# Kernel tuning notes

Measured on AMD Instinct MI355X. Metric: run time of the kernel, lower is better.

Reference implementation:

```python
import jax, jax.numpy as jnp
import numpy as np


def _lstm_dir(x_tbd, Wx, Wh, b, reverse):
    # x_tbd: [T, B, D]; Wx: [D, 4H]; Wh: [H, 4H]; b: [4H]
    if reverse:
        x_tbd = x_tbd[::-1]
    pre = jnp.einsum('tbd,dk->tbk', x_tbd, Wx) + b  # precompute input projection
    T, B, _ = x_tbd.shape
    H = Wh.shape[0]
    init = (jnp.zeros((B, H), x_tbd.dtype), jnp.zeros((B, H), x_tbd.dtype))

    def step(carry, zt):
        c, h = carry
        z = zt + h @ Wh  # [B, 4H]
        i, f, g, o = jnp.split(z, 4, axis=-1)
        i = jax.nn.sigmoid(i)
        f = jax.nn.sigmoid(f)
        g = jnp.tanh(g)
        o = jax.nn.sigmoid(o)
        c = f * c + i * g
        h = o * jnp.tanh(c)
        return (c, h), h

    _, hs = jax.lax.scan(step, init, pre)  # hs: [T, B, H]
    if reverse:
        hs = hs[::-1]
    return hs


def _bilstm(x, layers):
    # x: [B, T, D] batch-major -> time-major
    x = jnp.swapaxes(x, 0, 1)  # [T, B, D]
    for (Wxf, Whf, bf, Wxb, Whb, bb) in layers:
        hf = _lstm_dir(x, Wxf, Whf, bf, reverse=False)
        hb = _lstm_dir(x, Wxb, Whb, bb, reverse=True)
        x = jnp.concatenate([hf, hb], axis=-1)  # [T, B, 2H]
    return jnp.swapaxes(x, 0, 1)  # [B, T, 2H]


def setup_inputs() -> dict:
    key = jax.random.key(0)
    B, T, D, H = 8, 2048, 512, 512
    ks = jax.random.split(key, 9)
    s_in = 1.0 / np.sqrt(D)
    s_h = 1.0 / np.sqrt(H)
    s_in2 = 1.0 / np.sqrt(2 * H)
    return {
        'x': jax.random.normal(ks[0], (B, T, D), jnp.float32),
        'Wx0f': jax.random.normal(ks[1], (D, 4 * H), jnp.float32) * s_in,
        'Wh0f': jax.random.normal(ks[2], (H, 4 * H), jnp.float32) * s_h,
        'b0f': jnp.zeros((4 * H,), jnp.float32),
        'Wx0b': jax.random.normal(ks[3], (D, 4 * H), jnp.float32) * s_in,
        'Wh0b': jax.random.normal(ks[4], (H, 4 * H), jnp.float32) * s_h,
        'b0b': jnp.zeros((4 * H,), jnp.float32),
        'Wx1f': jax.random.normal(ks[5], (2 * H, 4 * H), jnp.float32) * s_in2,
        'Wh1f': jax.random.normal(ks[6], (H, 4 * H), jnp.float32) * s_h,
        'b1f': jnp.zeros((4 * H,), jnp.float32),
        'Wx1b': jax.random.normal(ks[7], (2 * H, 4 * H), jnp.float32) * s_in2,
        'Wh1b': jax.random.normal(ks[8], (H, 4 * H), jnp.float32) * s_h,
        'b1b': jnp.zeros((4 * H,), jnp.float32),
    }


def reference(x, Wx0f, Wh0f, b0f, Wx0b, Wh0b, b0b, Wx1f, Wh1f, b1f, Wx1b, Wh1b, b1b):
    layers = [
        (Wx0f, Wh0f, b0f, Wx0b, Wh0b, b0b),
        (Wx1f, Wh1f, b1f, Wx1b, Wh1b, b1b),
    ]
    return _bilstm(x, layers)
```

## Files before the change

### kernel.cpp

```cpp
#include <hip/hip_runtime.h>
#include <hip/hip_bf16.h>
#include <stdint.h>

typedef unsigned short u16;
typedef unsigned int   u32;
typedef unsigned long long u64;
typedef __attribute__((ext_vector_type(8))) short short8;
typedef __attribute__((ext_vector_type(4))) float f32x4;

#define T_SEQ 2048
#define NTOK  16384
#define NGATE 4096

__device__ __forceinline__ u16 f2bf(float f) {
    u32 u = __builtin_bit_cast(u32, f);
    return (u16)((u + 0x7fffu + ((u >> 16) & 1u)) >> 16);
}
__device__ __forceinline__ float bf2f(u16 s) {
    return __builtin_bit_cast(float, (u32)s << 16);
}

__device__ __forceinline__ void load2_sc0(const u64* p0, const u64* p1, u64& a, u64& b) {
    asm volatile("global_load_dwordx2 %0, %2, off sc0\n\t"
                 "global_load_dwordx2 %1, %3, off sc0\n\t"
                 "s_waitcnt vmcnt(0)"
                 : "=&v"(a), "=&v"(b)
                 : "v"(p0), "v"(p1)
                 : "memory");
}
__device__ __forceinline__ void store_sc0(u32* p, u32 v) {
    asm volatile("global_store_dword %0, %1, off sc0" :: "v"(p), "v"(v) : "memory");
}

__global__ void k_init(u32* comm, int n_comm) {
    int i = blockIdx.x * blockDim.x + threadIdx.x;
    int stride = gridDim.x * blockDim.x;
    for (int k = i; k < n_comm; k += stride) comm[k] = 0u;
}

__global__ void k_f2bf(const float* __restrict__ src, u16* __restrict__ dst, int n4) {
    int i = blockIdx.x * blockDim.x + threadIdx.x;
    if (i >= n4) return;
    float4 v = ((const float4*)src)[i];
    u32 lo = (u32)f2bf(v.x) | ((u32)f2bf(v.y) << 16);
    u32 hi = (u32)f2bf(v.z) | ((u32)f2bf(v.w) << 16);
    ((uint2*)dst)[i] = make_uint2(lo, hi);
}

__global__ void k_pack_wxT(const float* __restrict__ Wf, const float* __restrict__ Wb,
                           u16* __restrict__ dst, int K, int klog ) {
    int gid = blockIdx.x * blockDim.x + threadIdx.x;
    if (gid >= (NGATE << klog)) return;
    int n  = gid >> klog;
    int kc = gid & ((1 << klog) - 1);
    int dir = n >> 11, pcol = n & 2047;
    int c = pcol >> 4, uu = (pcol >> 2) & 3, g = pcol & 3;
    int u = c * 4 + uu;
    int oc = g * 512 + u;
    const float* src = dir ? Wb : Wf;
    u16* d = dst + (size_t)n * K + kc * 8;
    #pragma unroll
    for (int j = 0; j < 8; j++) d[j] = f2bf(src[(size_t)(kc * 8 + j) * 2048 + oc]);
}

__global__ void k_pack_whF(const float* __restrict__ Whf, const float* __restrict__ Whb,
                           u16* __restrict__ dst) {
    int gid = blockIdx.x * blockDim.x + threadIdx.x;
    int lane = gid & 63, kk = (gid >> 6) & 15, c = (gid >> 10) & 127, dir = (gid >> 17) & 1;
    int col16 = lane & 15, uu = col16 >> 2, g = col16 & 3;
    int u = c * 4 + uu, oc = g * 512 + u;
    int kbase = kk * 32 + (lane >> 4) * 8;
    const float* src = dir ? Whb : Whf;
    u16* d = dst + (size_t)gid * 8;
    #pragma unroll
    for (int j = 0; j < 8; j++) d[j] = f2bf(src[(size_t)(kbase + j) * 2048 + oc]);
}

template <int K>
__global__ __launch_bounds__(256) void k_gemm(const u16* __restrict__ A,
                                              const u16* __restrict__ BT,
                                              u16* __restrict__ C) {
    __shared__ __align__(16) u16 a_lds[128][72];
    __shared__ __align__(16) u16 b_lds[128][72];
    const int tid = threadIdx.x;
    const int lane = tid & 63;
    const int wav = tid >> 6;
    const int wr = wav >> 1, wc = wav & 1;
    const int row0 = blockIdx.y * 128, col0 = blockIdx.x * 128;
    const int r_ld = lane & 15;
    const int k_ld = (lane >> 4) * 8;
    f32x4 acc[4][4] = {};
    for (int kt = 0; kt < K; kt += 64) {
        __syncthreads();
        #pragma unroll
        for (int it = 0; it < 4; it++) {
            int cc = tid + it * 256;
            int r = cc >> 3, ko = (cc & 7) * 8;
            *(short8*)&a_lds[r][ko] = *(const short8*)&A[(size_t)(row0 + r) * K + kt + ko];
            *(short8*)&b_lds[r][ko] = *(const short8*)&BT[(size_t)(col0 + r) * K + kt + ko];
        }
        __syncthreads();
        #pragma unroll
        for (int kk = 0; kk < 2; kk++) {
            short8 af[4], bfr[4];
            #pragma unroll
            for (int m = 0; m < 4; m++)
                af[m] = *(const short8*)&a_lds[wr * 64 + m * 16 + r_ld][kk * 32 + k_ld];
            #pragma unroll
            for (int n = 0; n < 4; n++)
                bfr[n] = *(const short8*)&b_lds[wc * 64 + n * 16 + r_ld][kk * 32 + k_ld];
            #pragma unroll
            for (int m = 0; m < 4; m++)
                #pragma unroll
                for (int n = 0; n < 4; n++)
                    acc[m][n] = __builtin_amdgcn_mfma_f32_16x16x32_bf16(af[m], bfr[n], acc[m][n], 0, 0, 0);
        }
    }
    const int rrow = (lane >> 4) * 4;
    const int rcol = lane & 15;
    #pragma unroll
    for (int m = 0; m < 4; m++)
        #pragma unroll
        for (int n = 0; n < 4; n++) {
            size_t rbase = (size_t)(row0 + wr * 64 + m * 16 + rrow);
            int col = col0 + wc * 64 + n * 16 + rcol;
            #pragma unroll
            for (int r = 0; r < 4; r++)
                C[(rbase + r) * NGATE + col] = f2bf(acc[m][n][r]);
        }
}

__global__ __launch_bounds__(1024) void k_scan(
    const u16* __restrict__ pre,
    const u16* __restrict__ whF,
    const float* __restrict__ bias_f, const float* __restrict__ bias_b,
    u16* __restrict__ y_bf,
    float* __restrict__ y_f32,
    u32* __restrict__ commL,
    u32* __restrict__ commF)
{
    const int xcd = (int)(blockIdx.x & 7);
    if (xcd > 1) return;
    const int dir = xcd;
    const int p   = (int)(blockIdx.x >> 3);

    __shared__ __align__(16) u16   h_lds[2][8][520];
    __shared__ __align__(16) u16   z_pre[2][8][264];
    __shared__ __align__(16) float z_mm[2][8][260];

    const int tid = threadIdx.x;
    const int l   = tid & 63;
    const int w   = tid >> 6;

    short8 bfrag[16];
    {
        const u16* base = whF + (size_t)(dir * 128 + p * 16 + w) * 8192 + (size_t)l * 8;
        #pragma unroll
        for (int kk = 0; kk < 16; kk++) bfrag[kk] = *(const short8*)(base + kk * 512);
    }

    float c_st = 0.f;
    float bi = 0.f, bff = 0.f, bg = 0.f, bo = 0.f;
    const int gj  = tid & 63;
    const int u_g = p * 64 + gj;
    if (tid < 512) {
        const float* bias = dir ? bias_b : bias_f;
        bi  = bias[u_g];        bff = bias[512 + u_g];
        bg  = bias[1024 + u_g]; bo  = bias[1536 + u_g];
    }
    const int a_b = l & 7;
    const int a_k = (l >> 4) * 8;
    const int zr  = l >> 4;

    u32* const cbL = commL + (size_t)dir * 8192;
    u32* const cbF = commF + (size_t)dir * 8192;
    const int sb_b0 = tid >> 8;
    const int sb_u  = (2 * tid) & 511;

    for (int s = 0; s < T_SEQ; s++) {
        const int t  = dir ? (T_SEQ - 1 - s) : s;
        const int hb = s & 1;
        short8 preg;
        if (tid < 256) {
            int b = tid >> 5, seg = tid & 31;
            preg = *(const short8*)&pre[((size_t)b * T_SEQ + t) * NGATE + dir * 2048 + p * 256 + seg * 8];
        }
        asm volatile("" ::: "memory");
        {
            const u64* sbL = (const u64*)(cbL + (size_t)((s + 1) & 1) * 4096);
            const u64* sbF = (const u64*)(cbF + (size_t)((s + 1) & 1) * 4096);
            const u32 want = (u32)s & 0xffffu;
            u32 W0 = 0, W1 = 0, W2 = 0, W3 = 0;
            bool D0 = false, D1 = false, D2 = false, D3 = false;
            do {
                u64 l0 = __hip_atomic_load(&sbL[tid],        __ATOMIC_RELAXED, __HIP_MEMORY_SCOPE_AGENT);
                u64 l1 = __hip_atomic_load(&sbL[tid + 1024], __ATOMIC_RELAXED, __HIP_MEMORY_SCOPE_AGENT);
                u64 f0, f1;
                load2_sc0(&sbF[tid], &sbF[tid + 1024], f0, f1);
                if (!D0) { u32 a = (u32)f0;         u32 b = (u32)l0;
                           if ((a >> 16) == want) { W0 = a; D0 = true; }
                           else if ((b >> 16) == want) { W0 = b; D0 = true; } }
                if (!D1) { u32 a = (u32)(f0 >> 32); u32 b = (u32)(l0 >> 32);
                           if ((a >> 16) == want) { W1 = a; D1 = true; }
                           else if ((b >> 16) == want) { W1 = b; D1 = true; } }
                if (!D2) { u32 a = (u32)f1;         u32 b = (u32)l1;
                           if ((a >> 16) == want) { W2 = a; D2 = true; }
                           else if ((b >> 16) == want) { W2 = b; D2 = true; } }
                if (!D3) { u32 a = (u32)(f1 >> 32); u32 b = (u32)(l1 >> 32);
                           if ((a >> 16) == want) { W3 = a; D3 = true; }
                           else if ((b >> 16) == want) { W3 = b; D3 = true; } }
            } while (!(D0 && D1 && D2 && D3));
            *(u32*)&h_lds[hb][sb_b0][sb_u]     = (W0 & 0xffffu) | (W1 << 16);
            *(u32*)&h_lds[hb][sb_b0 + 4][sb_u] = (W2 & 0xffffu) | (W3 << 16);
        }
        if (tid < 256) {
            int b = tid >> 5, seg = tid & 31;
            *(short8*)&z_pre[hb][b][seg * 8] = preg;
        }
        __syncthreads();
        {
            f32x4 acc0 = {}, acc1 = {};
            #pragma unroll
            for (int kk = 0; kk < 8; kk++) {
                short8 a0 = *(const short8*)&h_lds[hb][a_b][kk * 32 + a_k];
                acc0 = __builtin_amdgcn_mfma_f32_16x16x32_bf16(a0, bfrag[kk], acc0, 0, 0, 0);
                short8 a1 = *(const short8*)&h_lds[hb][a_b][(kk + 8) * 32 + a_k];
                acc1 = __builtin_amdgcn_mfma_f32_16x16x32_bf16(a1, bfrag[kk + 8], acc1, 0, 0, 0);
            }
            if (zr < 2) {
                #pragma unroll
                for (int r = 0; r < 4; r++)
                    z_mm[hb][zr * 4 + r][w * 16 + (l & 15)] = acc0[r] + acc1[r];
            }
        }
        __syncthreads();
        if (tid < 512) {
            float4 z4 = *(const float4*)&z_mm[hb][w][4 * gj];
            u64 pz    = *(const u64*)&z_pre[hb][w][4 * gj];
            float zi = z4.x + bf2f((u16)pz)         + bi;
            float zf = z4.y + bf2f((u16)(pz >> 16)) + bff;
            float zg = z4.z + bf2f((u16)(pz >> 32)) + bg;
            float zo = z4.w + bf2f((u16)(pz >> 48)) + bo;
            float ig = 1.f / (1.f + __expf(-zi));
            float fg = 1.f / (1.f + __expf(-zf));
            float gg = 2.f / (1.f + __expf(-2.f * zg)) - 1.f;
            float og = 1.f / (1.f + __expf(-zo));
            c_st = fg * c_st + ig * gg;
            float th = 2.f / (1.f + __expf(-2.f * c_st)) - 1.f;
            float hv = og * th;
            u16 hb16 = f2bf(hv);
            u32 pw = (u32)hb16 | ((u32)((s + 1) & 0xffff) << 16);
            u32 idx = (u32)((s & 1) * 4096 + w * 512 + u_g);
            store_sc0(&cbF[idx], pw);
            __hip_atomic_store(&cbL[idx], pw, __ATOMIC_RELAXED, __HIP_MEMORY_SCOPE_AGENT);
            size_t rr = (size_t)w * T_SEQ + t;
            if (y_bf) y_bf[rr * 1024 + dir * 512 + u_g] = hb16;
            else      y_f32[rr * 1024 + dir * 512 + u_g] = hv;
        }
    }
}

extern "C" void kernel_launch(void* const* d_in, const int* in_sizes, int n_in,
                              void* d_out, int out_size, void* d_ws, size_t ws_size,
                              hipStream_t stream) {
    const float* x    = (const float*)d_in[0];
    const float* Wx0f = (const float*)d_in[1];
    const float* Wh0f = (const float*)d_in[2];
    const float* b0f  = (const float*)d_in[3];
    const float* Wx0b = (const float*)d_in[4];
    const float* Wh0b = (const float*)d_in[5];
    const float* b0b  = (const float*)d_in[6];
    const float* Wx1f = (const float*)d_in[7];
    const float* Wh1f = (const float*)d_in[8];
    const float* b1f  = (const float*)d_in[9];
    const float* Wx1b = (const float*)d_in[10];
    const float* Wh1b = (const float*)d_in[11];
    const float* b1b  = (const float*)d_in[12];
    float* out = (float*)d_out;

    char* ws = (char*)d_ws;
    size_t off = 0;
    auto take = [&](size_t bytes) {
        char* pp = ws + off;
        off = (off + bytes + 255) & ~(size_t)255;
        return pp;
    };
    u16* pre  = (u16*)take((size_t)NTOK * NGATE * 2);
    u16* x_bf = (u16*)take((size_t)NTOK * 512 * 2);
    u16* y0   = (u16*)take((size_t)NTOK * 1024 * 2);
    u16* wxT0 = (u16*)take((size_t)NGATE * 512 * 2);
    u16* wxT1 = (u16*)take((size_t)NGATE * 1024 * 2);
    u16* whF  = (u16*)take((size_t)2 * 2097152 * 2);
    u32* comm = (u32*)take((size_t)8 * 8192 * 4);

    u32* commL = comm;
    u32* commF = comm + 4 * 8192;

    k_init<<<32, 256, 0, stream>>>(comm, 8 * 8192);
    k_f2bf<<<8192, 256, 0, stream>>>(x, x_bf, NTOK * 512 / 4);
    k_pack_wxT<<<1024, 256, 0, stream>>>(Wx0f, Wx0b, wxT0, 512, 6);
    k_pack_wxT<<<2048, 256, 0, stream>>>(Wx1f, Wx1b, wxT1, 1024, 7);
    k_pack_whF<<<1024, 256, 0, stream>>>(Wh0f, Wh0b, whF);
    k_pack_whF<<<1024, 256, 0, stream>>>(Wh1f, Wh1b, whF + 2097152);

    k_gemm<512><<<dim3(32, 128), 256, 0, stream>>>(x_bf, wxT0, pre);
    k_scan<<<64, 1024, 0, stream>>>(pre, whF, b0f, b0b, y0, nullptr,
                                    commL, commF);
    k_gemm<1024><<<dim3(32, 128), 256, 0, stream>>>(y0, wxT1, pre);
    k_scan<<<64, 1024, 0, stream>>>(pre, whF + 2097152, b1f, b1b, nullptr, out,
                                    commL + 2 * 8192, commF + 2 * 8192);
}
```

Before: 11.99 ms.

## Split polling onto dedicated stager waves and poll mostly the sc0 buffer

Threads 512 to 1023 become dedicated stager waves. They alone poll the cross-block hidden-state exchange buffers and stage the precomputed gate inputs into LDS, while the lower threads handle gate math. Polling now reads four dwordx2 words per thread from the sc0 buffer each iteration and checks the atomic buffer only every 16th iteration. A pair of packed values counts as ready only when both halves carry the current step tag. The aim is to cut spin-loop memory traffic and take the exchange latency off the compute waves, at the cost of possibly slower detection when only the atomic copy is up to date.

```diff
diff --git a/kernel.cpp b/kernel.cpp
--- a/kernel.cpp
+++ b/kernel.cpp
@@ -20,12 +20,16 @@
     return __builtin_bit_cast(float, (u32)s << 16);
 }
 
-__device__ __forceinline__ void load2_sc0(const u64* p0, const u64* p1, u64& a, u64& b) {
-    asm volatile("global_load_dwordx2 %0, %2, off sc0\n\t"
-                 "global_load_dwordx2 %1, %3, off sc0\n\t"
+__device__ __forceinline__ void load4_sc0(const u64* p0, const u64* p1,
+                                          const u64* p2, const u64* p3,
+                                          u64& a, u64& b, u64& c, u64& d) {
+    asm volatile("global_load_dwordx2 %0, %4, off sc0\n\t"
+                 "global_load_dwordx2 %1, %5, off sc0\n\t"
+                 "global_load_dwordx2 %2, %6, off sc0\n\t"
+                 "global_load_dwordx2 %3, %7, off sc0\n\t"
                  "s_waitcnt vmcnt(0)"
-                 : "=&v"(a), "=&v"(b)
-                 : "v"(p0), "v"(p1)
+                 : "=&v"(a), "=&v"(b), "=&v"(c), "=&v"(d)
+                 : "v"(p0), "v"(p1), "v"(p2), "v"(p3)
                  : "memory");
 }
 __device__ __forceinline__ void store_sc0(u32* p, u32 v) {
@@ -151,6 +155,8 @@
     const int tid = threadIdx.x;
     const int l   = tid & 63;
     const int w   = tid >> 6;
+    const bool stager = (tid >= 512);
+    const int tidp = tid & 511;
 
     short8 bfrag[16];
     {
@@ -163,7 +169,7 @@
     float bi = 0.f, bff = 0.f, bg = 0.f, bo = 0.f;
     const int gj  = tid & 63;
     const int u_g = p * 64 + gj;
-    if (tid < 512) {
+    if (!stager) {
         const float* bias = dir ? bias_b : bias_f;
         bi  = bias[u_g];        bff = bias[512 + u_g];
         bg  = bias[1024 + u_g]; bo  = bias[1536 + u_g];
@@ -174,48 +180,56 @@
 
     u32* const cbL = commL + (size_t)dir * 8192;
     u32* const cbF = commF + (size_t)dir * 8192;
-    const int sb_b0 = tid >> 8;
-    const int sb_u  = (2 * tid) & 511;
 
     for (int s = 0; s < T_SEQ; s++) {
         const int t  = dir ? (T_SEQ - 1 - s) : s;
         const int hb = s & 1;
-        short8 preg;
-        if (tid < 256) {
-            int b = tid >> 5, seg = tid & 31;
-            preg = *(const short8*)&pre[((size_t)b * T_SEQ + t) * NGATE + dir * 2048 + p * 256 + seg * 8];
-        }
-        asm volatile("" ::: "memory");
-        {
-            const u64* sbL = (const u64*)(cbL + (size_t)((s + 1) & 1) * 4096);
-            const u64* sbF = (const u64*)(cbF + (size_t)((s + 1) & 1) * 4096);
-            const u32 want = (u32)s & 0xffffu;
-            u32 W0 = 0, W1 = 0, W2 = 0, W3 = 0;
-            bool D0 = false, D1 = false, D2 = false, D3 = false;
-            do {
-                u64 l0 = __hip_atomic_load(&sbL[tid],        __ATOMIC_RELAXED, __HIP_MEMORY_SCOPE_AGENT);
-                u64 l1 = __hip_atomic_load(&sbL[tid + 1024], __ATOMIC_RELAXED, __HIP_MEMORY_SCOPE_AGENT);
-                u64 f0, f1;
-                load2_sc0(&sbF[tid], &sbF[tid + 1024], f0, f1);
-                if (!D0) { u32 a = (u32)f0;         u32 b = (u32)l0;
-                           if ((a >> 16) == want) { W0 = a; D0 = true; }
-                           else if ((b >> 16) == want) { W0 = b; D0 = true; } }
-                if (!D1) { u32 a = (u32)(f0 >> 32); u32 b = (u32)(l0 >> 32);
-                           if ((a >> 16) == want) { W1 = a; D1 = true; }
-                           else if ((b >> 16) == want) { W1 = b; D1 = true; } }
-                if (!D2) { u32 a = (u32)f1;         u32 b = (u32)l1;
-                           if ((a >> 16) == want) { W2 = a; D2 = true; }
-                           else if ((b >> 16) == want) { W2 = b; D2 = true; } }
-                if (!D3) { u32 a = (u32)(f1 >> 32); u32 b = (u32)(l1 >> 32);
-                           if ((a >> 16) == want) { W3 = a; D3 = true; }
-                           else if ((b >> 16) == want) { W3 = b; D3 = true; } }
-            } while (!(D0 && D1 && D2 && D3));
-            *(u32*)&h_lds[hb][sb_b0][sb_u]     = (W0 & 0xffffu) | (W1 << 16);
-            *(u32*)&h_lds[hb][sb_b0 + 4][sb_u] = (W2 & 0xffffu) | (W3 << 16);
-        }
-        if (tid < 256) {
-            int b = tid >> 5, seg = tid & 31;
-            *(short8*)&z_pre[hb][b][seg * 8] = preg;
+        if (stager) {
+            short8 preg;
+            if (tid < 768) {
+                int b = tidp >> 5, seg = tid & 31;
+                preg = *(const short8*)&pre[((size_t)b * T_SEQ + t) * NGATE + dir * 2048 + p * 256 + seg * 8];
+            }
+            asm volatile("" ::: "memory");
+            {
+                const u64* sbF = (const u64*)(cbF + (size_t)((s + 1) & 1) * 4096);
+                const u64* sbL = (const u64*)(cbL + (size_t)((s + 1) & 1) * 4096);
+                const u32 want = (u32)s & 0xffffu;
+                u32 w0 = 0, w1 = 0, w2 = 0, w3 = 0;
+                bool d0 = false, d1 = false, d2 = false, d3 = false;
+                auto chk = [&](u64 f, u32& wq, bool& dq) {
+                    if (!dq) {
+                        u32 lo = (u32)f, hi = (u32)(f >> 32);
+                        if (((lo >> 16) == want) & ((hi >> 16) == want)) {
+                            wq = (lo & 0xffffu) | (hi << 16); dq = true;
+                        }
+                    }
+                };
+                int it = 0;
+                for (;;) {
+                    u64 f0, f1, f2, f3;
+                    load4_sc0(&sbF[tidp], &sbF[tidp + 512], &sbF[tidp + 1024], &sbF[tidp + 1536],
+                              f0, f1, f2, f3);
+                    chk(f0, w0, d0); chk(f1, w1, d1); chk(f2, w2, d2); chk(f3, w3, d3);
+                    if (d0 & d1 & d2 & d3) break;
+                    if (((++it) & 15) == 0) {
+                        u64 g0 = __hip_atomic_load(&sbL[tidp],        __ATOMIC_RELAXED, __HIP_MEMORY_SCOPE_AGENT);
+                        u64 g1 = __hip_atomic_load(&sbL[tidp + 512],  __ATOMIC_RELAXED, __HIP_MEMORY_SCOPE_AGENT);
+                        u64 g2 = __hip_atomic_load(&sbL[tidp + 1024], __ATOMIC_RELAXED, __HIP_MEMORY_SCOPE_AGENT);
+                        u64 g3 = __hip_atomic_load(&sbL[tidp + 1536], __ATOMIC_RELAXED, __HIP_MEMORY_SCOPE_AGENT);
+                        chk(g0, w0, d0); chk(g1, w1, d1); chk(g2, w2, d2); chk(g3, w3, d3);
+                        if (d0 & d1 & d2 & d3) break;
+                    }
+                }
+                *(u32*)&h_lds[hb][(tidp >> 8) + 0][((tidp & 255) * 2)] = w0;
+                *(u32*)&h_lds[hb][(tidp >> 8) + 2][((tidp & 255) * 2)] = w1;
+                *(u32*)&h_lds[hb][(tidp >> 8) + 4][((tidp & 255) * 2)] = w2;
+                *(u32*)&h_lds[hb][(tidp >> 8) + 6][((tidp & 255) * 2)] = w3;
+            }
+            if (tid < 768) {
+                int b = tidp >> 5, seg = tid & 31;
+                *(short8*)&z_pre[hb][b][seg * 8] = preg;
+            }
         }
         __syncthreads();
         {
@@ -234,7 +248,7 @@
             }
         }
         __syncthreads();
-        if (tid < 512) {
+        if (!stager) {
             float4 z4 = *(const float4*)&z_mm[hb][w][4 * gj];
             u64 pz    = *(const u64*)&z_pre[hb][w][4 * gj];
             float zi = z4.x + bf2f((u16)pz)         + bi;
```

Measured after the change: 30.50 ms. 154% more time.

## Co-locate both scan directions on one XCD via runtime election and prefetch pre

Applied to the files above, without the earlier changes.

The scan kernel now launches 128 blocks and reads the hardware XCC id. The first XCD to gather 16 blocks wins an atomic election, and both directions (16 workgroups) run on that single XCD. The intent is to keep the h-exchange traffic within one XCD's cache rather than spreading it across two XCDs. The poll loop now checks the fast (sc0) buffer every iteration and the L2-coherent buffer only every fourth iteration, and the next timestep's pre-activation load is issued one step ahead. Both directions now share one XCD's compute units and cache, which may add contention, and the election spin adds startup cost.

```diff
diff --git a/kernel.cpp b/kernel.cpp
--- a/kernel.cpp
+++ b/kernel.cpp
@@ -18,6 +18,11 @@
 }
 __device__ __forceinline__ float bf2f(u16 s) {
     return __builtin_bit_cast(float, (u32)s << 16);
+}
+__device__ __forceinline__ int get_xcc_id() {
+    u32 x;
+    asm volatile("s_getreg_b32 %0, hwreg(HW_REG_XCC_ID)" : "=s"(x));
+    return (int)(x & 7u);
 }
 
 __device__ __forceinline__ void load2_sc0(const u64* p0, const u64* p1, u64& a, u64& b) {
@@ -32,10 +37,11 @@
     asm volatile("global_store_dword %0, %1, off sc0" :: "v"(p), "v"(v) : "memory");
 }
 
-__global__ void k_init(u32* comm, int n_comm) {
+__global__ void k_init(u32* comm, int n_comm, int* elect, int n_elect) {
     int i = blockIdx.x * blockDim.x + threadIdx.x;
     int stride = gridDim.x * blockDim.x;
     for (int k = i; k < n_comm; k += stride) comm[k] = 0u;
+    for (int k = i; k < n_elect; k += stride) elect[k] = ((k & 15) == 8) ? -1 : 0;
 }
 
 __global__ void k_f2bf(const float* __restrict__ src, u16* __restrict__ dst, int n4) {
@@ -137,18 +143,38 @@
     u16* __restrict__ y_bf,
     float* __restrict__ y_f32,
     u32* __restrict__ commL,
-    u32* __restrict__ commF)
+    u32* __restrict__ commF,
+    int* __restrict__ elect)
 {
-    const int xcd = (int)(blockIdx.x & 7);
-    if (xcd > 1) return;
-    const int dir = xcd;
-    const int p   = (int)(blockIdx.x >> 3);
+    __shared__ int s_role;
+    const int tid = threadIdx.x;
+    if (tid == 0) {
+        int xcd = get_xcc_id();
+        int role = -1;
+        int r = __hip_atomic_fetch_add(&elect[xcd], 1, __ATOMIC_RELAXED, __HIP_MEMORY_SCOPE_AGENT);
+        if (r < 16) {
+            if (r == 15) {
+                int exp = -1;
+                __hip_atomic_compare_exchange_strong(&elect[8], &exp, xcd,
+                    __ATOMIC_RELEASE, __ATOMIC_RELAXED, __HIP_MEMORY_SCOPE_AGENT);
+            }
+            int wnr;
+            while ((wnr = __hip_atomic_load(&elect[8], __ATOMIC_ACQUIRE, __HIP_MEMORY_SCOPE_AGENT)) < 0)
+                __builtin_amdgcn_s_sleep(8);
+            if (wnr == xcd) role = r;
+        }
+        s_role = role;
+    }
+    __syncthreads();
+    const int role = s_role;
+    if (role < 0) return;
+    const int dir = role >> 3;
+    const int p   = role & 7;
 
     __shared__ __align__(16) u16   h_lds[2][8][520];
     __shared__ __align__(16) u16   z_pre[2][8][264];
     __shared__ __align__(16) float z_mm[2][8][260];
 
-    const int tid = threadIdx.x;
     const int l   = tid & 63;
     const int w   = tid >> 6;
 
@@ -177,45 +203,49 @@
     const int sb_b0 = tid >> 8;
     const int sb_u  = (2 * tid) & 511;
 
+    const int pr_b = tid >> 5, pr_seg = tid & 31;
+    short8 preg;
+    if (tid < 256) {
+        const int t0 = dir ? (T_SEQ - 1) : 0;
+        preg = *(const short8*)&pre[((size_t)pr_b * T_SEQ + t0) * NGATE + dir * 2048 + p * 256 + pr_seg * 8];
+    }
+
     for (int s = 0; s < T_SEQ; s++) {
         const int t  = dir ? (T_SEQ - 1 - s) : s;
         const int hb = s & 1;
-        short8 preg;
-        if (tid < 256) {
-            int b = tid >> 5, seg = tid & 31;
-            preg = *(const short8*)&pre[((size_t)b * T_SEQ + t) * NGATE + dir * 2048 + p * 256 + seg * 8];
-        }
-        asm volatile("" ::: "memory");
         {
+            const u64* sbF = (const u64*)(cbF + (size_t)((s + 1) & 1) * 4096);
             const u64* sbL = (const u64*)(cbL + (size_t)((s + 1) & 1) * 4096);
-            const u64* sbF = (const u64*)(cbF + (size_t)((s + 1) & 1) * 4096);
             const u32 want = (u32)s & 0xffffu;
             u32 W0 = 0, W1 = 0, W2 = 0, W3 = 0;
             bool D0 = false, D1 = false, D2 = false, D3 = false;
-            do {
-                u64 l0 = __hip_atomic_load(&sbL[tid],        __ATOMIC_RELAXED, __HIP_MEMORY_SCOPE_AGENT);
-                u64 l1 = __hip_atomic_load(&sbL[tid + 1024], __ATOMIC_RELAXED, __HIP_MEMORY_SCOPE_AGENT);
+            auto chk = [&](u32 v, u32& W, bool& D) {
+                if (!D && ((v >> 16) == want)) { W = v; D = true; }
+            };
+            int it = 0;
+            for (;;) {
                 u64 f0, f1;
                 load2_sc0(&sbF[tid], &sbF[tid + 1024], f0, f1);
-                if (!D0) { u32 a = (u32)f0;         u32 b = (u32)l0;
-                           if ((a >> 16) == want) { W0 = a; D0 = true; }
-                           else if ((b >> 16) == want) { W0 = b; D0 = true; } }
-                if (!D1) { u32 a = (u32)(f0 >> 32); u32 b = (u32)(l0 >> 32);
-                           if ((a >> 16) == want) { W1 = a; D1 = true; }
-                           else if ((b >> 16) == want) { W1 = b; D1 = true; } }
-                if (!D2) { u32 a = (u32)f1;         u32 b = (u32)l1;
-                           if ((a >> 16) == want) { W2 = a; D2 = true; }
-                           else if ((b >> 16) == want) { W2 = b; D2 = true; } }
-                if (!D3) { u32 a = (u32)(f1 >> 32); u32 b = (u32)(l1 >> 32);
-                           if ((a >> 16) == want) { W3 = a; D3 = true; }
-                           else if ((b >> 16) == want) { W3 = b; D3 = true; } }
-            } while (!(D0 && D1 && D2 && D3));
-            *(u32*)&h_lds[hb][sb_b0][sb_u]     = (W0 & 0xffffu) | (W1 << 16);
+                chk((u32)f0, W0, D0); chk((u32)(f0 >> 32), W1, D1);
+                chk((u32)f1, W2, D2); chk((u32)(f1 >> 32), W3, D3);
+                if (D0 & D1 & D2 & D3) break;
+                if (((++it) & 3) == 0) {
+                    u64 l0 = __hip_atomic_load(&sbL[tid],        __ATOMIC_RELAXED, __HIP_MEMORY_SCOPE_AGENT);
+                    u64 l1 = __hip_atomic_load(&sbL[tid + 1024], __ATOMIC_RELAXED, __HIP_MEMORY_SCOPE_AGENT);
+                    chk((u32)l0, W0, D0); chk((u32)(l0 >> 32), W1, D1);
+                    chk((u32)l1, W2, D2); chk((u32)(l1 >> 32), W3, D3);
+                    if (D0 & D1 & D2 & D3) break;
+                }
+            }
+            *(u32*)&h_lds[hb][sb_b0 + 0][sb_u] = (W0 & 0xffffu) | (W1 << 16);
             *(u32*)&h_lds[hb][sb_b0 + 4][sb_u] = (W2 & 0xffffu) | (W3 << 16);
         }
         if (tid < 256) {
-            int b = tid >> 5, seg = tid & 31;
-            *(short8*)&z_pre[hb][b][seg * 8] = preg;
+            *(short8*)&z_pre[hb][pr_b][pr_seg * 8] = preg;
+            if (s + 1 < T_SEQ) {
+                const int t2 = dir ? (T_SEQ - 2 - s) : (s + 1);
+                preg = *(const short8*)&pre[((size_t)pr_b * T_SEQ + t2) * NGATE + dir * 2048 + p * 256 + pr_seg * 8];
+            }
         }
         __syncthreads();
         {
@@ -292,11 +322,12 @@
     u16* wxT1 = (u16*)take((size_t)NGATE * 1024 * 2);
     u16* whF  = (u16*)take((size_t)2 * 2097152 * 2);
     u32* comm = (u32*)take((size_t)8 * 8192 * 4);
+    int* elect = (int*)take((size_t)32 * 4);
 
     u32* commL = comm;
     u32* commF = comm + 4 * 8192;
 
-    k_init<<<32, 256, 0, stream>>>(comm, 8 * 8192);
+    k_init<<<32, 256, 0, stream>>>(comm, 8 * 8192, elect, 32);
     k_f2bf<<<8192, 256, 0, stream>>>(x, x_bf, NTOK * 512 / 4);
     k_pack_wxT<<<1024, 256, 0, stream>>>(Wx0f, Wx0b, wxT0, 512, 6);
     k_pack_wxT<<<2048, 256, 0, stream>>>(Wx1f, Wx1b, wxT1, 1024, 7);
@@ -304,9 +335,10 @@
     k_pack_whF<<<1024, 256, 0, stream>>>(Wh1f, Wh1b, whF + 2097152);
 
     k_gemm<512><<<dim3(32, 128), 256, 0, stream>>>(x_bf, wxT0, pre);
-    k_scan<<<64, 1024, 0, stream>>>(pre, whF, b0f, b0b, y0, nullptr,
-                                    commL, commF);
+    k_scan<<<128, 1024, 0, stream>>>(pre, whF, b0f, b0b, y0, nullptr,
+                                     commL, commF, elect);
     k_gemm<1024><<<dim3(32, 128), 256, 0, stream>>>(y0, wxT1, pre);
-    k_scan<<<64, 1024, 0, stream>>>(pre, whF + 2097152, b1f, b1b, nullptr, out,
-                                    commL + 2 * 8192, commF + 2 * 8192);
-}
+    k_scan<<<128, 1024, 0, stream>>>(pre, whF + 2097152, b1f, b1b, nullptr, out,
+                                     commL + 2 * 8192, commF + 2 * 8192,
+                                     elect + 16);
+}
```

Measured after the change: 15.44 ms. 28.7% more time.
